# Optimization experiments

Measured on AMD Instinct MI355X. Metric: run time of the kernel, lower is better.

The kernel has to match this reference:

```python
import jax, jax.numpy as jnp
import numpy as np

SCALE = 8.0  # sqrt(head_dim=64)
NEG = -1000000000.0

def setup_inputs() -> dict:
    key = jax.random.key(0)
    kq, kk, kv, km, kb = jax.random.split(key, 5)
    B, H, S, D = 4, 16, 2048, 64
    q = jax.random.normal(kq, (B, H, S, D), dtype=jnp.float32)
    k = jax.random.normal(kk, (B, H, S, D), dtype=jnp.float32)
    v = jax.random.normal(kv, (B, H, S, D), dtype=jnp.float32)
    mask = jax.random.randint(km, (B, 1, S, S), 0, 2, dtype=jnp.int32)
    bias = jax.random.normal(kb, (1, H, S, S), dtype=jnp.float32)
    return {"q": q, "k": k, "v": v, "mask": mask, "bias": bias}

def reference(q, k, v, mask, bias):
    # attn = (q/scale) @ k^T  -> [B, H, S, S]
    attn = jnp.einsum('bhqd,bhkd->bhqk', q / SCALE, k)
    attn = jnp.where(mask == 0, NEG, attn)
    attn = attn + bias
    attn = jax.nn.softmax(attn, axis=-1)
    # dropout is identity in eval/deterministic mode
    output = jnp.einsum('bhqk,bhkd->bhqd', attn, v)
    return (output, attn)
```

## Files before the change

kernel.cpp:

```cpp
#include <hip/hip_runtime.h>
#include <cstdint>
#include <cstddef>

constexpr int Bn = 4, Hn = 16, Sn = 2048, Dn = 64;
constexpr int TQ = 64;
constexpr int TK = 32;
constexpr int SW = Sn / 32;

typedef __attribute__((ext_vector_type(8))) short frag8;
typedef __attribute__((ext_vector_type(4))) float f32x4;

__device__ __forceinline__ short f2bf(float f) {
  unsigned u = __builtin_bit_cast(unsigned, f);
  u = (u + 0x7FFFu + ((u >> 16) & 1u)) >> 16;
  return (short)u;
}

__global__ void cast_bf16_kernel(const float* __restrict__ in,
                                 short* __restrict__ out, float scale, int n4) {
  int i = blockIdx.x * blockDim.x + threadIdx.x;
  if (i >= n4) return;
  float4 v = ((const float4*)in)[i];
  short4 o;
  o.x = f2bf(v.x * scale);
  o.y = f2bf(v.y * scale);
  o.z = f2bf(v.z * scale);
  o.w = f2bf(v.w * scale);
  ((short4*)out)[i] = o;
}

__global__ void transpose_v_kernel(const float* __restrict__ v,
                                   short* __restrict__ vt) {
  __shared__ short tile[64][65];
  int bh = blockIdx.x >> 5;
  int s0 = (blockIdx.x & 31) * 64;
  const float* src = v + ((size_t)bh * Sn + s0) * Dn;
  short* dst = vt + (size_t)bh * Dn * Sn;
  int t = threadIdx.x;
  int col = t & 63, r0 = t >> 6;
  for (int r = r0; r < 64; r += 4) tile[r][col] = f2bf(src[r * Dn + col]);
  __syncthreads();
  int sl = t & 63, d0 = t >> 6;
  for (int d = d0; d < 64; d += 4) dst[(size_t)d * Sn + s0 + sl] = tile[sl][d];
}

__global__ void pack_mask_kernel(const int* __restrict__ m,
                                 unsigned* __restrict__ out) {
  int i = blockIdx.x * blockDim.x + threadIdx.x;
  unsigned long long bal = __ballot(m[i] != 0);
  int lane = threadIdx.x & 63;
  if (lane == 0)
    out[i >> 5] = (unsigned)bal;
  else if (lane == 32)
    out[i >> 5] = (unsigned)(bal >> 32);
}

__global__ __launch_bounds__(256, 8) void attn_kernel(
    const short* __restrict__ qbf, const short* __restrict__ kbf,
    const short* __restrict__ vtbf, const unsigned* __restrict__ maskp,
    const float* __restrict__ bias, float* __restrict__ outO,
    float* __restrict__ outA) {
  int gid = blockIdx.x;
  int b = gid & 3;
  int h = (gid >> 2) & 15;
  int qt = gid >> 6;
  int bh = b * Hn + h;
  int wave = threadIdx.x >> 6;
  int lane = threadIdx.x & 63;
  int l16 = lane & 15;
  int quad = lane >> 4;
  int q0 = qt * TQ + wave * 16;

  const short* Q = qbf + (size_t)bh * Sn * Dn;
  const short* K = kbf + (size_t)bh * Sn * Dn;
  const short* VT = vtbf + (size_t)bh * Dn * Sn;
  const unsigned* Mp = maskp + (size_t)b * Sn * SW;
  const float* Bi = bias + (size_t)h * Sn * Sn;
  float* Oo = outO + (size_t)bh * Sn * Dn;
  float* Ao = outA + (size_t)bh * Sn * Sn;

  frag8 qa0 = *(const frag8*)(Q + (q0 + l16) * Dn + quad * 8);
  frag8 qa1 = *(const frag8*)(Q + (q0 + l16) * Dn + 32 + quad * 8);

  float lsum[4] = {0.f, 0.f, 0.f, 0.f};
  for (int kt = 0; kt < Sn; kt += TK) {
    frag8 kb0a = *(const frag8*)(K + (kt + l16) * Dn + quad * 8);
    frag8 kb1a = *(const frag8*)(K + (kt + l16) * Dn + 32 + quad * 8);
    frag8 kb0b = *(const frag8*)(K + (kt + 16 + l16) * Dn + quad * 8);
    frag8 kb1b = *(const frag8*)(K + (kt + 16 + l16) * Dn + 32 + quad * 8);
    f32x4 s0 = {0.f, 0.f, 0.f, 0.f};
    f32x4 s1 = {0.f, 0.f, 0.f, 0.f};
    s0 = __builtin_amdgcn_mfma_f32_16x16x32_bf16(qa0, kb0a, s0, 0, 0, 0);
    s0 = __builtin_amdgcn_mfma_f32_16x16x32_bf16(qa1, kb1a, s0, 0, 0, 0);
    s1 = __builtin_amdgcn_mfma_f32_16x16x32_bf16(qa0, kb0b, s1, 0, 0, 0);
    s1 = __builtin_amdgcn_mfma_f32_16x16x32_bf16(qa1, kb1b, s1, 0, 0, 0);
    int kw = kt >> 5;
#pragma unroll
    for (int r = 0; r < 4; ++r) {
      int row = q0 + quad * 4 + r;
      unsigned mw = Mp[(size_t)row * SW + kw];
      const float* brow = Bi + (size_t)row * Sn + kt + l16;
      float t0 = ((mw >> l16) & 1u) ? s0[r] + brow[0] : -1e9f;
      float t1 = ((mw >> (16 + l16)) & 1u) ? s1[r] + brow[16] : -1e9f;
      lsum[r] += __expf(t0) + __expf(t1);
    }
  }
  float inv[4];
#pragma unroll
  for (int r = 0; r < 4; ++r) {
    float v = lsum[r];
    v += __shfl_xor(v, 1);
    v += __shfl_xor(v, 2);
    v += __shfl_xor(v, 4);
    v += __shfl_xor(v, 8);
    inv[r] = 1.0f / v;
  }

  __shared__ short plds[4][16][40];
  f32x4 oacc[4];
#pragma unroll
  for (int d = 0; d < 4; ++d) oacc[d] = (f32x4){0.f, 0.f, 0.f, 0.f};

  for (int kt = 0; kt < Sn; kt += TK) {
    frag8 kb0a = *(const frag8*)(K + (kt + l16) * Dn + quad * 8);
    frag8 kb1a = *(const frag8*)(K + (kt + l16) * Dn + 32 + quad * 8);
    frag8 kb0b = *(const frag8*)(K + (kt + 16 + l16) * Dn + quad * 8);
    frag8 kb1b = *(const frag8*)(K + (kt + 16 + l16) * Dn + 32 + quad * 8);
    f32x4 s0 = {0.f, 0.f, 0.f, 0.f};
    f32x4 s1 = {0.f, 0.f, 0.f, 0.f};
    s0 = __builtin_amdgcn_mfma_f32_16x16x32_bf16(qa0, kb0a, s0, 0, 0, 0);
    s0 = __builtin_amdgcn_mfma_f32_16x16x32_bf16(qa1, kb1a, s0, 0, 0, 0);
    s1 = __builtin_amdgcn_mfma_f32_16x16x32_bf16(qa0, kb0b, s1, 0, 0, 0);
    s1 = __builtin_amdgcn_mfma_f32_16x16x32_bf16(qa1, kb1b, s1, 0, 0, 0);
    int kw = kt >> 5;
#pragma unroll
    for (int r = 0; r < 4; ++r) {
      int row = q0 + quad * 4 + r;
      unsigned mw = Mp[(size_t)row * SW + kw];
      size_t off = (size_t)row * Sn + kt + l16;
      float p0 = ((mw >> l16) & 1u) ? __expf(s0[r] + Bi[off]) * inv[r] : 0.f;
      float p1 =
          ((mw >> (16 + l16)) & 1u) ? __expf(s1[r] + Bi[off + 16]) * inv[r] : 0.f;
      Ao[off] = p0;
      Ao[off + 16] = p1;
      plds[wave][quad * 4 + r][l16] = f2bf(p0);
      plds[wave][quad * 4 + r][16 + l16] = f2bf(p1);
    }
    frag8 pa = *(const frag8*)(&plds[wave][l16][quad * 8]);
#pragma unroll
    for (int d = 0; d < 4; ++d) {
      frag8 vb =
          *(const frag8*)(VT + (size_t)(d * 16 + l16) * Sn + kt + quad * 8);
      oacc[d] = __builtin_amdgcn_mfma_f32_16x16x32_bf16(pa, vb, oacc[d], 0, 0, 0);
    }
  }

#pragma unroll
  for (int d = 0; d < 4; ++d)
#pragma unroll
    for (int r = 0; r < 4; ++r)
      Oo[(size_t)(q0 + quad * 4 + r) * Dn + d * 16 + l16] = oacc[d][r];
}

extern "C" void kernel_launch(void* const* d_in, const int* in_sizes, int n_in,
                              void* d_out, int out_size, void* d_ws,
                              size_t ws_size, hipStream_t stream) {
  const float* q = (const float*)d_in[0];
  const float* k = (const float*)d_in[1];
  const float* v = (const float*)d_in[2];
  const int* mask = (const int*)d_in[3];
  const float* bias = (const float*)d_in[4];

  float* outO = (float*)d_out;
  float* outA = outO + (size_t)Bn * Hn * Sn * Dn;

  const size_t nqk = (size_t)Bn * Hn * Sn * Dn;
  short* qbf = (short*)d_ws;
  short* kbf = qbf + nqk;
  short* vtbf = kbf + nqk;
  unsigned* maskp = (unsigned*)(vtbf + nqk);

  int n4 = (int)(nqk / 4);
  cast_bf16_kernel<<<(n4 + 255) / 256, 256, 0, stream>>>(q, qbf, 0.125f, n4);
  cast_bf16_kernel<<<(n4 + 255) / 256, 256, 0, stream>>>(k, kbf, 1.0f, n4);
  transpose_v_kernel<<<Bn * Hn * (Sn / 64), 256, 0, stream>>>(v, vtbf);
  int nm = Bn * Sn * Sn;
  pack_mask_kernel<<<nm / 256, 256, 0, stream>>>(mask, maskp);
  attn_kernel<<<Bn * Hn * Sn / TQ, 256, 0, stream>>>(qbf, kbf, vtbf, maskp,
                                                     bias, outO, outA);
}
```

Baseline: 2.383 ms.

## Software-prefetch K, mask and bias one tile ahead in both attention passes

Both key-loop passes now load the next tile's K fragments, packed mask words and bias values into registers while the current tile is computed, rotating them at the end of each iteration. The V fragments are also issued before the QK MFMAs in the second pass. Launch bounds are relaxed from 8 to 4 blocks per CU so the extra live registers fit. This hides global load latency at the cost of higher register pressure and possibly lower occupancy.

```diff
diff --git a/kernel.cpp b/kernel.cpp
--- a/kernel.cpp
+++ b/kernel.cpp
@@ -55,7 +55,7 @@
     out[i >> 5] = (unsigned)(bal >> 32);
 }
 
-__global__ __launch_bounds__(256, 8) void attn_kernel(
+__global__ __launch_bounds__(256, 4) void attn_kernel(
     const short* __restrict__ qbf, const short* __restrict__ kbf,
     const short* __restrict__ vtbf, const unsigned* __restrict__ maskp,
     const float* __restrict__ bias, float* __restrict__ outO,
@@ -82,27 +82,62 @@
   frag8 qa0 = *(const frag8*)(Q + (q0 + l16) * Dn + quad * 8);
   frag8 qa1 = *(const frag8*)(Q + (q0 + l16) * Dn + 32 + quad * 8);
 
+  size_t mrow[4], brow[4];
+#pragma unroll
+  for (int r = 0; r < 4; ++r) {
+    int row = q0 + quad * 4 + r;
+    mrow[r] = (size_t)row * SW;
+    brow[r] = (size_t)row * Sn;
+  }
+
   float lsum[4] = {0.f, 0.f, 0.f, 0.f};
-  for (int kt = 0; kt < Sn; kt += TK) {
-    frag8 kb0a = *(const frag8*)(K + (kt + l16) * Dn + quad * 8);
-    frag8 kb1a = *(const frag8*)(K + (kt + l16) * Dn + 32 + quad * 8);
-    frag8 kb0b = *(const frag8*)(K + (kt + 16 + l16) * Dn + quad * 8);
-    frag8 kb1b = *(const frag8*)(K + (kt + 16 + l16) * Dn + 32 + quad * 8);
-    f32x4 s0 = {0.f, 0.f, 0.f, 0.f};
-    f32x4 s1 = {0.f, 0.f, 0.f, 0.f};
-    s0 = __builtin_amdgcn_mfma_f32_16x16x32_bf16(qa0, kb0a, s0, 0, 0, 0);
-    s0 = __builtin_amdgcn_mfma_f32_16x16x32_bf16(qa1, kb1a, s0, 0, 0, 0);
-    s1 = __builtin_amdgcn_mfma_f32_16x16x32_bf16(qa0, kb0b, s1, 0, 0, 0);
-    s1 = __builtin_amdgcn_mfma_f32_16x16x32_bf16(qa1, kb1b, s1, 0, 0, 0);
-    int kw = kt >> 5;
+  {
+    frag8 k0a = *(const frag8*)(K + l16 * Dn + quad * 8);
+    frag8 k1a = *(const frag8*)(K + l16 * Dn + 32 + quad * 8);
+    frag8 k0b = *(const frag8*)(K + (16 + l16) * Dn + quad * 8);
+    frag8 k1b = *(const frag8*)(K + (16 + l16) * Dn + 32 + quad * 8);
+    unsigned mc[4];
+    float bc0[4], bc1[4];
 #pragma unroll
     for (int r = 0; r < 4; ++r) {
-      int row = q0 + quad * 4 + r;
-      unsigned mw = Mp[(size_t)row * SW + kw];
-      const float* brow = Bi + (size_t)row * Sn + kt + l16;
-      float t0 = ((mw >> l16) & 1u) ? s0[r] + brow[0] : -1e9f;
-      float t1 = ((mw >> (16 + l16)) & 1u) ? s1[r] + brow[16] : -1e9f;
-      lsum[r] += __expf(t0) + __expf(t1);
+      mc[r] = Mp[mrow[r]];
+      bc0[r] = Bi[brow[r] + l16];
+      bc1[r] = Bi[brow[r] + 16 + l16];
+    }
+    for (int kt = 0; kt < Sn; kt += TK) {
+      int nkt = (kt + TK) & (Sn - 1);
+      frag8 n0a = *(const frag8*)(K + (nkt + l16) * Dn + quad * 8);
+      frag8 n1a = *(const frag8*)(K + (nkt + l16) * Dn + 32 + quad * 8);
+      frag8 n0b = *(const frag8*)(K + (nkt + 16 + l16) * Dn + quad * 8);
+      frag8 n1b = *(const frag8*)(K + (nkt + 16 + l16) * Dn + 32 + quad * 8);
+      unsigned mn[4];
+      float bn0[4], bn1[4];
+      int nkw = nkt >> 5;
+#pragma unroll
+      for (int r = 0; r < 4; ++r) {
+        mn[r] = Mp[mrow[r] + nkw];
+        bn0[r] = Bi[brow[r] + nkt + l16];
+        bn1[r] = Bi[brow[r] + nkt + 16 + l16];
+      }
+      f32x4 s0 = {0.f, 0.f, 0.f, 0.f};
+      f32x4 s1 = {0.f, 0.f, 0.f, 0.f};
+      s0 = __builtin_amdgcn_mfma_f32_16x16x32_bf16(qa0, k0a, s0, 0, 0, 0);
+      s0 = __builtin_amdgcn_mfma_f32_16x16x32_bf16(qa1, k1a, s0, 0, 0, 0);
+      s1 = __builtin_amdgcn_mfma_f32_16x16x32_bf16(qa0, k0b, s1, 0, 0, 0);
+      s1 = __builtin_amdgcn_mfma_f32_16x16x32_bf16(qa1, k1b, s1, 0, 0, 0);
+#pragma unroll
+      for (int r = 0; r < 4; ++r) {
+        float t0 = ((mc[r] >> l16) & 1u) ? s0[r] + bc0[r] : -1e9f;
+        float t1 = ((mc[r] >> (16 + l16)) & 1u) ? s1[r] + bc1[r] : -1e9f;
+        lsum[r] += __expf(t0) + __expf(t1);
+      }
+      k0a = n0a; k1a = n1a; k0b = n0b; k1b = n1b;
+#pragma unroll
+      for (int r = 0; r < 4; ++r) {
+        mc[r] = mn[r];
+        bc0[r] = bn0[r];
+        bc1[r] = bn1[r];
+      }
     }
   }
   float inv[4];
@@ -121,37 +156,69 @@
 #pragma unroll
   for (int d = 0; d < 4; ++d) oacc[d] = (f32x4){0.f, 0.f, 0.f, 0.f};
 
-  for (int kt = 0; kt < Sn; kt += TK) {
-    frag8 kb0a = *(const frag8*)(K + (kt + l16) * Dn + quad * 8);
-    frag8 kb1a = *(const frag8*)(K + (kt + l16) * Dn + 32 + quad * 8);
-    frag8 kb0b = *(const frag8*)(K + (kt + 16 + l16) * Dn + quad * 8);
-    frag8 kb1b = *(const frag8*)(K + (kt + 16 + l16) * Dn + 32 + quad * 8);
-    f32x4 s0 = {0.f, 0.f, 0.f, 0.f};
-    f32x4 s1 = {0.f, 0.f, 0.f, 0.f};
-    s0 = __builtin_amdgcn_mfma_f32_16x16x32_bf16(qa0, kb0a, s0, 0, 0, 0);
-    s0 = __builtin_amdgcn_mfma_f32_16x16x32_bf16(qa1, kb1a, s0, 0, 0, 0);
-    s1 = __builtin_amdgcn_mfma_f32_16x16x32_bf16(qa0, kb0b, s1, 0, 0, 0);
-    s1 = __builtin_amdgcn_mfma_f32_16x16x32_bf16(qa1, kb1b, s1, 0, 0, 0);
-    int kw = kt >> 5;
+  {
+    frag8 k0a = *(const frag8*)(K + l16 * Dn + quad * 8);
+    frag8 k1a = *(const frag8*)(K + l16 * Dn + 32 + quad * 8);
+    frag8 k0b = *(const frag8*)(K + (16 + l16) * Dn + quad * 8);
+    frag8 k1b = *(const frag8*)(K + (16 + l16) * Dn + 32 + quad * 8);
+    unsigned mc[4];
+    float bc0[4], bc1[4];
 #pragma unroll
     for (int r = 0; r < 4; ++r) {
-      int row = q0 + quad * 4 + r;
-      unsigned mw = Mp[(size_t)row * SW + kw];
-      size_t off = (size_t)row * Sn + kt + l16;
-      float p0 = ((mw >> l16) & 1u) ? __expf(s0[r] + Bi[off]) * inv[r] : 0.f;
-      float p1 =
-          ((mw >> (16 + l16)) & 1u) ? __expf(s1[r] + Bi[off + 16]) * inv[r] : 0.f;
-      Ao[off] = p0;
-      Ao[off + 16] = p1;
-      plds[wave][quad * 4 + r][l16] = f2bf(p0);
-      plds[wave][quad * 4 + r][16 + l16] = f2bf(p1);
-    }
-    frag8 pa = *(const frag8*)(&plds[wave][l16][quad * 8]);
-#pragma unroll
-    for (int d = 0; d < 4; ++d) {
-      frag8 vb =
-          *(const frag8*)(VT + (size_t)(d * 16 + l16) * Sn + kt + quad * 8);
-      oacc[d] = __builtin_amdgcn_mfma_f32_16x16x32_bf16(pa, vb, oacc[d], 0, 0, 0);
+      mc[r] = Mp[mrow[r]];
+      bc0[r] = Bi[brow[r] + l16];
+      bc1[r] = Bi[brow[r] + 16 + l16];
+    }
+    for (int kt = 0; kt < Sn; kt += TK) {
+      int nkt = (kt + TK) & (Sn - 1);
+      frag8 n0a = *(const frag8*)(K + (nkt + l16) * Dn + quad * 8);
+      frag8 n1a = *(const frag8*)(K + (nkt + l16) * Dn + 32 + quad * 8);
+      frag8 n0b = *(const frag8*)(K + (nkt + 16 + l16) * Dn + quad * 8);
+      frag8 n1b = *(const frag8*)(K + (nkt + 16 + l16) * Dn + 32 + quad * 8);
+      unsigned mn[4];
+      float bn0[4], bn1[4];
+      int nkw = nkt >> 5;
+#pragma unroll
+      for (int r = 0; r < 4; ++r) {
+        mn[r] = Mp[mrow[r] + nkw];
+        bn0[r] = Bi[brow[r] + nkt + l16];
+        bn1[r] = Bi[brow[r] + nkt + 16 + l16];
+      }
+      frag8 vb0 = *(const frag8*)(VT + (size_t)(l16)*Sn + kt + quad * 8);
+      frag8 vb1 = *(const frag8*)(VT + (size_t)(16 + l16) * Sn + kt + quad * 8);
+      frag8 vb2 = *(const frag8*)(VT + (size_t)(32 + l16) * Sn + kt + quad * 8);
+      frag8 vb3 = *(const frag8*)(VT + (size_t)(48 + l16) * Sn + kt + quad * 8);
+      f32x4 s0 = {0.f, 0.f, 0.f, 0.f};
+      f32x4 s1 = {0.f, 0.f, 0.f, 0.f};
+      s0 = __builtin_amdgcn_mfma_f32_16x16x32_bf16(qa0, k0a, s0, 0, 0, 0);
+      s0 = __builtin_amdgcn_mfma_f32_16x16x32_bf16(qa1, k1a, s0, 0, 0, 0);
+      s1 = __builtin_amdgcn_mfma_f32_16x16x32_bf16(qa0, k0b, s1, 0, 0, 0);
+      s1 = __builtin_amdgcn_mfma_f32_16x16x32_bf16(qa1, k1b, s1, 0, 0, 0);
+#pragma unroll
+      for (int r = 0; r < 4; ++r) {
+        size_t off = brow[r] + kt + l16;
+        float p0 =
+            ((mc[r] >> l16) & 1u) ? __expf(s0[r] + bc0[r]) * inv[r] : 0.f;
+        float p1 = ((mc[r] >> (16 + l16)) & 1u)
+                       ? __expf(s1[r] + bc1[r]) * inv[r]
+                       : 0.f;
+        Ao[off] = p0;
+        Ao[off + 16] = p1;
+        plds[wave][quad * 4 + r][l16] = f2bf(p0);
+        plds[wave][quad * 4 + r][16 + l16] = f2bf(p1);
+      }
+      frag8 pa = *(const frag8*)(&plds[wave][l16][quad * 8]);
+      oacc[0] = __builtin_amdgcn_mfma_f32_16x16x32_bf16(pa, vb0, oacc[0], 0, 0, 0);
+      oacc[1] = __builtin_amdgcn_mfma_f32_16x16x32_bf16(pa, vb1, oacc[1], 0, 0, 0);
+      oacc[2] = __builtin_amdgcn_mfma_f32_16x16x32_bf16(pa, vb2, oacc[2], 0, 0, 0);
+      oacc[3] = __builtin_amdgcn_mfma_f32_16x16x32_bf16(pa, vb3, oacc[3], 0, 0, 0);
+      k0a = n0a; k1a = n1a; k0b = n0b; k1b = n1b;
+#pragma unroll
+      for (int r = 0; r < 4; ++r) {
+        mc[r] = mn[r];
+        bc0[r] = bn0[r];
+        bc1[r] = bn1[r];
+      }
     }
   }
 
```

New measurement: 2.136 ms. -10.4%, faster.
